# Kernel tuning notes

Measured on AMD Instinct MI355X. Metric: run time of the kernel, lower is better.

The kernel has to match this reference:

```python
import jax, jax.numpy as jnp
import numpy as np

N_NODES = 50000
N_EDGES = 800000
D = 128          # input_dim == output_dim
H = 2 * D        # hidden size = 2*output_dim
EPS = 1e-5       # BatchNorm1d eps


def _mlp(x, W1, b1, g1, beta1, W2, b2):
    # Linear -> BatchNorm1d (training-mode batch stats) -> ReLU -> Linear
    y = x @ W1 + b1
    mu = jnp.mean(y, axis=0)
    var = jnp.mean(jnp.square(y - mu), axis=0)  # biased var, as used for normalization
    y = (y - mu) * jax.lax.rsqrt(var + EPS) * g1 + beta1
    y = jax.nn.relu(y)
    return y @ W2 + b2


def setup_inputs() -> dict:
    key = jax.random.key(0)
    ks = jax.random.split(key, 16)
    h = jax.random.normal(ks[0], (N_NODES, D), dtype=jnp.float32)
    e = jax.random.normal(ks[1], (N_EDGES, D), dtype=jnp.float32)
    src = jax.random.randint(ks[2], (N_EDGES,), 0, N_NODES, dtype=jnp.int32)
    dst = jax.random.randint(ks[3], (N_EDGES,), 0, N_NODES, dtype=jnp.int32)

    def lin(k, fan_in, fan_out):
        return jax.random.normal(k, (fan_in, fan_out), dtype=jnp.float32) * (1.0 / np.sqrt(fan_in))

    params = {
        # mlp_bond: in 2D -> H -> D
        'W1b': lin(ks[4], 2 * D, H), 'b1b': jnp.zeros((H,), jnp.float32),
        'g1b': jnp.ones((H,), jnp.float32), 'beta1b': jnp.zeros((H,), jnp.float32),
        'W2b': lin(ks[5], H, D), 'b2b': jnp.zeros((D,), jnp.float32),
        # mlp_atom: in 2D -> H -> D
        'W1a': lin(ks[6], 2 * D, H), 'b1a': jnp.zeros((H,), jnp.float32),
        'g1a': jnp.ones((H,), jnp.float32), 'beta1a': jnp.zeros((H,), jnp.float32),
        'W2a': lin(ks[7], H, D), 'b2a': jnp.zeros((D,), jnp.float32),
    }
    return {'h': h, 'e': e, 'src': src, 'dst': dst, **params}


def reference(h, e, src, dst,
              W1b, b1b, g1b, beta1b, W2b, b2b,
              W1a, b1a, g1a, beta1a, W2a, b2a):
    # --- bond update: gather u_add_v, concat with e, MLP ---
    sum_h_edge = h[src] + h[dst]                              # [E, D]
    e_new = _mlp(jnp.concatenate([sum_h_edge, e], axis=-1),
                 W1b, b1b, g1b, beta1b, W2b, b2b)             # [E, D]

    # --- atom update: scatter-sum of src node feats and NEW edge feats to dst ---
    sum_h = jax.ops.segment_sum(h[src], dst, num_segments=N_NODES)   # copy_u + sum
    sum_e = jax.ops.segment_sum(e_new, dst, num_segments=N_NODES)   # copy_e + sum
    h_new = _mlp(jnp.concatenate([sum_h, sum_e], axis=-1),
                 W1a, b1a, g1a, beta1a, W2a, b2a)             # [N, D]

    # out_batch_norm=False, out_activation=None, residual=False, dropout=None
    return h_new, e_new
```

## Files before the change

### kernel.cpp

```cpp
#include <hip/hip_runtime.h>
#include <hip/hip_bf16.h>
#include <stdint.h>

#define DD 128
#define HH 256
#define EPSBN 1e-5f

typedef __attribute__((ext_vector_type(4))) float f32x4;
typedef __attribute__((ext_vector_type(8))) short s16x8;
typedef __attribute__((ext_vector_type(4))) short s16x4;

__device__ __forceinline__ unsigned short f2bf(float f){
  union { __hip_bfloat16 h; unsigned short u; } v;
  v.h = __float2bfloat16(f);
  return v.u;
}
__device__ __forceinline__ float bf2f(unsigned short s){
  union{unsigned u; float f;} v; v.u=((unsigned)s)<<16; return v.f;
}
__device__ __forceinline__ int swz(int row, int kb){ return row*512 + (kb ^ ((row&31)<<4)); }

__global__ void wt_kernel(const float* __restrict__ W1b, const float* __restrict__ W2b,
                          const float* __restrict__ W1a, const float* __restrict__ W2a,
                          unsigned short* __restrict__ WT1b, unsigned short* __restrict__ WT2b,
                          unsigned short* __restrict__ WT1a, unsigned short* __restrict__ WT2a){
  int idx = blockIdx.x*256 + threadIdx.x;
  if (idx < 65536){ int n=idx>>8, k=idx&255; WT1b[n*256+k]=f2bf(W1b[k*256+n]); }
  else if (idx < 98304){ int t=idx-65536; int n=t>>8, k=t&255; WT2b[n*256+k]=f2bf(W2b[k*128+n]); }
  else if (idx < 163840){ int t=idx-98304; int n=t>>8, k=t&255; WT1a[n*256+k]=f2bf(W1a[k*256+n]); }
  else if (idx < 196608){ int t=idx-163840; int n=t>>8, k=t&255; WT2a[n*256+k]=f2bf(W2a[k*128+n]); }
}

__global__ void h2bf_hist_kernel(const float* __restrict__ h, unsigned short* __restrict__ hb, int n8,
                                 const int* __restrict__ dst, int* __restrict__ counts, int E){
  int i = blockIdx.x*256 + threadIdx.x;
  if (i < n8){
    f32x4 a = *(const f32x4*)(h + (size_t)i*8);
    f32x4 b = *(const f32x4*)(h + (size_t)i*8 + 4);
    s16x8 p;
    #pragma unroll
    for (int q=0;q<4;q++){ p[q]=(short)f2bf(a[q]); p[4+q]=(short)f2bf(b[q]); }
    *(s16x8*)(hb + (size_t)i*8) = p;
  }
  if (i < E) atomicAdd(&counts[dst[i]], 1);
}

__global__ void scan_kernel(const int* __restrict__ counts, int* __restrict__ offsets,
                            int* __restrict__ cursor, int n){
  __shared__ int wsum[16];
  int tid = threadIdx.x, lane = tid&63, wid = tid>>6;
  int carry = 0;
  int nch = (n + 1023)/1024;
  for (int ch=0; ch<nch; ch++){
    int i = ch*1024 + tid;
    int v = (i<n)? counts[i] : 0;
    int s = v;
    #pragma unroll
    for (int off=1; off<64; off<<=1){ int t = __shfl_up(s, off); if (lane>=off) s += t; }
    if (lane==63) wsum[wid] = s;
    __syncthreads();
    int woff = 0, tot = 0;
    #pragma unroll
    for (int w=0; w<16; w++){ int t = wsum[w]; if (w<wid) woff += t; tot += t; }
    if (i<n){ int excl = carry + woff + s - v; offsets[i]=excl; cursor[i]=excl; }
    carry += tot;
    __syncthreads();
  }
  if (tid==0) offsets[n] = carry;
}

__global__ void fill_kernel(const int* __restrict__ dst, const int* __restrict__ srcv,
                            int* __restrict__ cursor,
                            int* __restrict__ eids, int* __restrict__ esrc, int E){
  int i = blockIdx.x*256 + threadIdx.x;
  if (i < E){
    int slot = atomicAdd(&cursor[dst[i]], 1);
    eids[slot] = i;
    esrc[slot] = srcv[i];
  }
}

__device__ __forceinline__ void gemm1_core(char* xt, const s16x8 (&Bf)[8][2],
                                           float bias0, float bias1,
                                           unsigned short* __restrict__ yout,
                                           float* __restrict__ stats,
                                           int base, int nrows)
{
  const int tid = threadIdx.x;
  const int l = tid&63, w = tid>>6, lr = l&15, lg = l>>4;
  const int nb = w*32;
  f32x4 acc[4][2];
  #pragma unroll
  for (int mt=0;mt<4;mt++)
    #pragma unroll
    for (int nt=0;nt<2;nt++) acc[mt][nt] = (f32x4){0.f,0.f,0.f,0.f};
  #pragma unroll
  for (int kc=0;kc<8;kc++){
    s16x8 af[4];
    #pragma unroll
    for (int mt=0;mt<4;mt++)
      af[mt] = *(const s16x8*)(xt + swz(mt*16 + lr, kc*64 + lg*16));
    #pragma unroll
    for (int nt=0;nt<2;nt++)
      #pragma unroll
      for (int mt=0;mt<4;mt++)
        acc[mt][nt] = __builtin_amdgcn_mfma_f32_16x16x32_bf16(af[mt], Bf[kc][nt], acc[mt][nt], 0,0,0);
  }
  float st1a=0.f, st1b=0.f, st2a=0.f, st2b=0.f;
  #pragma unroll
  for (int mt=0;mt<4;mt++)
    #pragma unroll
    for (int q=0;q<4;q++){
      float m = (base + mt*16 + lg*4 + q < nrows) ? 1.0f : 0.0f;
      float v0 = (acc[mt][0][q] + bias0)*m;
      float v1 = (acc[mt][1][q] + bias1)*m;
      st1a += v0; st2a += v0*v0;
      st1b += v1; st2b += v1*v1;
    }
  __syncthreads();
  #pragma unroll
  for (int mt=0;mt<4;mt++)
    #pragma unroll
    for (int q=0;q<4;q++){
      *(unsigned short*)(xt + (mt*16 + lg*4 + q)*512 + (nb + lr)*2)      = f2bf(acc[mt][0][q] + bias0);
      *(unsigned short*)(xt + (mt*16 + lg*4 + q)*512 + (nb + 16 + lr)*2) = f2bf(acc[mt][1][q] + bias1);
    }
  __syncthreads();
  #pragma unroll
  for (int it=0;it<4;it++){
    int off = it*8192 + tid*16;
    int row = off >> 9;
    if (base + row < nrows)
      *(s16x8*)((char*)yout + (size_t)base*512 + off) = *(const s16x8*)(xt + off);
  }
  {
    int rep = blockIdx.x & 63;
    float s;
    s = st1a; s += __shfl_xor(s,16); s += __shfl_xor(s,32);
    if (l < 16) atomicAdd(&stats[rep*512 + nb + lr], s);
    s = st2a; s += __shfl_xor(s,16); s += __shfl_xor(s,32);
    if (l < 16) atomicAdd(&stats[rep*512 + 256 + nb + lr], s);
    s = st1b; s += __shfl_xor(s,16); s += __shfl_xor(s,32);
    if (l < 16) atomicAdd(&stats[rep*512 + nb + 16 + lr], s);
    s = st2b; s += __shfl_xor(s,16); s += __shfl_xor(s,32);
    if (l < 16) atomicAdd(&stats[rep*512 + 256 + nb + 16 + lr], s);
  }
}

__global__ __launch_bounds__(512, 4) void edge_mlp1(
    const unsigned short* __restrict__ hb, const float* __restrict__ e,
    const int* __restrict__ src, const int* __restrict__ dstv,
    const unsigned short* __restrict__ WT1, const float* __restrict__ b1,
    unsigned short* __restrict__ yout, float* __restrict__ stats, int E)
{
  __shared__ alignas(16) char xt[32768];
  const int tid = threadIdx.x;
  const int l = tid&63, w = tid>>6, lr = l&15, lg = l>>4;
  const int nb = w*32;
  const int base = blockIdx.x*64;

  {
    const int cb = tid&31, r0 = tid>>5;
    #pragma unroll
    for (int k=0;k<4;k++){
      int r = r0 + k*16;
      f32x4 v = *(const f32x4*)(e + (size_t)(base+r)*DD + cb*4);
      s16x4 p;
      #pragma unroll
      for (int q=0;q<4;q++) p[q] = (short)f2bf(v[q]);
      *(s16x4*)(xt + swz(r, 256 + cb*8)) = p;
    }
  }
  {
    const int r = tid>>3, jj = tid&7;
    const int ei = base + r;
    int s_ = src[ei], d_ = dstv[ei];
    const s16x8* hs = (const s16x8*)(hb + (size_t)s_*DD) + jj*2;
    const s16x8* hd = (const s16x8*)(hb + (size_t)d_*DD) + jj*2;
    s16x8 a0=hs[0], a1=hs[1], c0=hd[0], c1=hd[1];
    s16x8 o0, o1;
    #pragma unroll
    for (int q=0;q<8;q++){
      o0[q] = (short)f2bf(bf2f((unsigned short)a0[q]) + bf2f((unsigned short)c0[q]));
      o1[q] = (short)f2bf(bf2f((unsigned short)a1[q]) + bf2f((unsigned short)c1[q]));
    }
    *(s16x8*)(xt + swz(r, jj*32))      = o0;
    *(s16x8*)(xt + swz(r, jj*32 + 16)) = o1;
  }
  s16x8 Bf[8][2];
  #pragma unroll
  for (int kc=0;kc<8;kc++)
    #pragma unroll
    for (int nt=0;nt<2;nt++)
      Bf[kc][nt] = *(const s16x8*)(WT1 + (size_t)(nb + nt*16 + lr)*256 + kc*32 + lg*8);
  float bias0 = b1[nb+lr], bias1 = b1[nb+16+lr];
  __syncthreads();
  gemm1_core(xt, Bf, bias0, bias1, yout, stats, base, E);
}

__global__ __launch_bounds__(256, 8) void node_gather(
    const unsigned short* __restrict__ hb, const float* __restrict__ enew,
    const int* __restrict__ offsets, const int* __restrict__ eids, const int* __restrict__ esrc,
    unsigned short* __restrict__ xnode, int NN)
{
  const int tid = threadIdx.x;
  const int r = tid>>3, jj = tid&7;
  const int node = blockIdx.x*32 + r;
  if (node >= NN) return;
  float ah[16], ae[16];
  #pragma unroll
  for (int q=0;q<16;q++){ ah[q]=0.f; ae[q]=0.f; }
  int beg = offsets[node], end = offsets[node+1];
  if (beg < end){
    int eid = eids[beg];
    int s_  = esrc[beg];
    for (int p = beg; p < end; p++){
      int pn = (p+1 < end) ? p+1 : p;
      int eid_n = eids[pn];
      int s_n   = esrc[pn];
      const s16x8* hs = (const s16x8*)(hb + (size_t)s_*DD + jj*16);
      const f32x4* ep = (const f32x4*)(enew + (size_t)eid*DD + jj*16);
      s16x8 a0 = hs[0], a1 = hs[1];
      f32x4 e0 = ep[0], e1 = ep[1], e2 = ep[2], e3 = ep[3];
      #pragma unroll
      for (int q=0;q<8;q++){ ah[q] += bf2f((unsigned short)a0[q]); ah[8+q] += bf2f((unsigned short)a1[q]); }
      #pragma unroll
      for (int q=0;q<4;q++){ ae[q] += e0[q]; ae[4+q] += e1[q]; ae[8+q] += e2[q]; ae[12+q] += e3[q]; }
      eid = eid_n; s_ = s_n;
    }
  }
  s16x8 o0, o1;
  #pragma unroll
  for (int q=0;q<8;q++){ o0[q] = (short)f2bf(ah[q]); o1[q] = (short)f2bf(ah[8+q]); }
  *(s16x8*)(xnode + (size_t)node*HH + jj*16)     = o0;
  *(s16x8*)(xnode + (size_t)node*HH + jj*16 + 8) = o1;
  #pragma unroll
  for (int q=0;q<8;q++){ o0[q] = (short)f2bf(ae[q]); o1[q] = (short)f2bf(ae[8+q]); }
  *(s16x8*)(xnode + (size_t)node*HH + 128 + jj*16)     = o0;
  *(s16x8*)(xnode + (size_t)node*HH + 128 + jj*16 + 8) = o1;
}

__global__ __launch_bounds__(512, 4) void node_gemm1(
    const unsigned short* __restrict__ xnode,
    const unsigned short* __restrict__ WT1, const float* __restrict__ b1,
    unsigned short* __restrict__ yout, float* __restrict__ stats, int NN)
{
  __shared__ alignas(16) char xt[32768];
  const int tid = threadIdx.x;
  const int l = tid&63, w = tid>>6, lr = l&15, lg = l>>4;
  const int nb = w*32;
  const int base = blockIdx.x*64;

  #pragma unroll
  for (int it=0;it<4;it++){
    int off = it*8192 + tid*16;
    int row = off >> 9, kb = off & 511;
    s16x8 v = {0,0,0,0,0,0,0,0};
    if (base + row < NN) v = *(const s16x8*)((const char*)xnode + (size_t)base*512 + off);
    *(s16x8*)(xt + swz(row, kb)) = v;
  }
  s16x8 Bf[8][2];
  #pragma unroll
  for (int kc=0;kc<8;kc++)
    #pragma unroll
    for (int nt=0;nt<2;nt++)
      Bf[kc][nt] = *(const s16x8*)(WT1 + (size_t)(nb + nt*16 + lr)*256 + kc*32 + lg*8);
  float bias0 = b1[nb+lr], bias1 = b1[nb+16+lr];
  __syncthreads();
  gemm1_core(xt, Bf, bias0, bias1, yout, stats, base, NN);
}

__global__ void finalize_kernel(const float* __restrict__ stats, const float* __restrict__ g,
                                const float* __restrict__ beta, float* __restrict__ scale, float invcnt){
  __shared__ float red[512];
  int tid = threadIdx.x;
  float s = 0.f;
  for (int rep=0; rep<64; rep++) s += stats[rep*512 + tid];
  red[tid] = s;
  __syncthreads();
  if (tid < 256){
    float mu  = red[tid]*invcnt;
    float var = red[256+tid]*invcnt - mu*mu;
    float a = g[tid] * rsqrtf(var + EPSBN);
    float c = beta[tid] - mu*a;
    scale[2*tid] = a; scale[2*tid+1] = c;
  }
}

__global__ __launch_bounds__(512, 4) void mlp2_kernel(const unsigned short* y,
    const unsigned short* __restrict__ WT2, const float* __restrict__ b2,
    const float* __restrict__ scale, float* outp, int nrows)
{
  __shared__ alignas(16) char xt[32768];
  const int tid = threadIdx.x;
  const int l = tid&63, w = tid>>6, lr = l&15, lg = l>>4;
  const int nb = w*16;
  const int base0 = blockIdx.x*128;

  s16x8 Bf[8];
  #pragma unroll
  for (int kc=0;kc<8;kc++)
    Bf[kc] = *(const s16x8*)(WT2 + (size_t)(nb + lr)*HH + kc*32 + lg*8);
  float bias = b2[nb+lr];
  const int cb = tid&31, r0 = tid>>5;
  float sa[8], sc[8];
  #pragma unroll
  for (int q=0;q<8;q++){ sa[q]=scale[2*(cb*8+q)]; sc[q]=scale[2*(cb*8+q)+1]; }

  #pragma unroll 1
  for (int t=0;t<2;t++){
    const int base = base0 + t*64;
    #pragma unroll
    for (int k=0;k<4;k++){
      int r = r0 + k*16;
      s16x8 raw = {0,0,0,0,0,0,0,0};
      if (base + r < nrows) raw = *(const s16x8*)(y + (size_t)(base+r)*HH + cb*8);
      s16x8 o;
      #pragma unroll
      for (int q=0;q<8;q++){
        float f = fmaxf(bf2f((unsigned short)raw[q])*sa[q] + sc[q], 0.0f);
        o[q] = (short)f2bf(f);
      }
      *(s16x8*)(xt + swz(r, cb*16)) = o;
    }
    __syncthreads();
    f32x4 acc[4];
    #pragma unroll
    for (int mt=0;mt<4;mt++) acc[mt] = (f32x4){0.f,0.f,0.f,0.f};
    #pragma unroll
    for (int kc=0;kc<8;kc++){
      s16x8 af[4];
      #pragma unroll
      for (int mt=0;mt<4;mt++)
        af[mt] = *(const s16x8*)(xt + swz(mt*16 + lr, kc*64 + lg*16));
      #pragma unroll
      for (int mt=0;mt<4;mt++)
        acc[mt] = __builtin_amdgcn_mfma_f32_16x16x32_bf16(af[mt], Bf[kc], acc[mt], 0,0,0);
    }
    __syncthreads();
    #pragma unroll
    for (int mt=0;mt<4;mt++)
      #pragma unroll
      for (int q=0;q<4;q++)
        *(float*)(xt + (mt*16 + lg*4 + q)*512 + (nb + lr)*4) = acc[mt][q] + bias;
    __syncthreads();
    #pragma unroll
    for (int it=0;it<4;it++){
      int off = it*8192 + tid*16;
      int row = off >> 9;
      if (base + row < nrows)
        *(f32x4*)(outp + (size_t)(base+row)*DD + ((off&511)>>2)) = *(const f32x4*)(xt + off);
    }
    if (t==0) __syncthreads();
  }
}

extern "C" void kernel_launch(void* const* d_in, const int* in_sizes, int n_in,
                              void* d_out, int out_size, void* d_ws, size_t ws_size,
                              hipStream_t stream) {
  const float* h    = (const float*)d_in[0];
  const float* e    = (const float*)d_in[1];
  const int*   src  = (const int*)d_in[2];
  const int*   dst  = (const int*)d_in[3];
  const float* W1b  = (const float*)d_in[4];
  const float* b1b  = (const float*)d_in[5];
  const float* g1b  = (const float*)d_in[6];
  const float* beta1b=(const float*)d_in[7];
  const float* W2b  = (const float*)d_in[8];
  const float* b2b  = (const float*)d_in[9];
  const float* W1a  = (const float*)d_in[10];
  const float* b1a  = (const float*)d_in[11];
  const float* g1a  = (const float*)d_in[12];
  const float* beta1a=(const float*)d_in[13];
  const float* W2a  = (const float*)d_in[14];
  const float* b2a  = (const float*)d_in[15];

  const int E  = in_sizes[2];
  const int NN = in_sizes[0] / DD;

  char* ws = (char*)d_ws;
  unsigned short* WT1b = (unsigned short*)(ws + 0);
  unsigned short* WT2b = (unsigned short*)(ws + 131072);
  unsigned short* WT1a = (unsigned short*)(ws + 196608);
  unsigned short* WT2a = (unsigned short*)(ws + 327680);
  float* scaleE = (float*)(ws + 393216);
  float* scaleN = (float*)(ws + 395264);
  float* statsE = (float*)(ws + 397312);
  float* statsN = (float*)(ws + 528384);
  int* counts  = (int*)(ws + 659456);
  int* offsets = (int*)(ws + 860160);
  int* cursor  = (int*)(ws + 1060864);
  int* eids    = (int*)(ws + 1261568);
  unsigned short* ya = (unsigned short*)(ws + 4461568);
  unsigned short* hb = (unsigned short*)(ws + 30086144);
  int* esrc   = (int*)(ws + 42886144);

  float* outH = (float*)d_out;
  float* outE = outH + (size_t)NN * DD;
  unsigned short* yE = (unsigned short*)outE;
  unsigned short* xnode = (unsigned short*)outH;

  hipMemsetAsync(ws + 397312, 0, 131072 + 131072 + 200704, stream);

  wt_kernel<<<768, 256, 0, stream>>>(W1b, W2b, W1a, W2a, WT1b, WT2b, WT1a, WT2a);
  h2bf_hist_kernel<<<(NN*DD/8 + 255)/256, 256, 0, stream>>>(h, hb, NN*DD/8, dst, counts, E);
  scan_kernel<<<1, 1024, 0, stream>>>(counts, offsets, cursor, NN);
  fill_kernel<<<(E+255)/256, 256, 0, stream>>>(dst, src, cursor, eids, esrc, E);

  const int tE64  = E/64;
  const int tE128 = E/128;
  const int tN64  = (NN + 63)/64;
  const int tN128 = (NN + 127)/128;
  const int gG    = (NN + 31)/32;

  edge_mlp1<<<tE64, 512, 0, stream>>>(hb, e, src, dst, WT1b, b1b, yE, statsE, E);
  finalize_kernel<<<1, 512, 0, stream>>>(statsE, g1b, beta1b, scaleE, 1.0f/(float)E);
  mlp2_kernel<<<tE128, 512, 0, stream>>>(yE, WT2b, b2b, scaleE, outE, E);
  node_gather<<<gG, 256, 0, stream>>>(hb, outE, offsets, eids, esrc, xnode, NN);
  node_gemm1<<<tN64, 512, 0, stream>>>(xnode, WT1a, b1a, ya, statsN, NN);
  finalize_kernel<<<1, 512, 0, stream>>>(statsN, g1a, beta1a, scaleN, 1.0f/(float)NN);
  mlp2_kernel<<<tN128, 512, 0, stream>>>(ya, WT2a, b2a, scaleN, outH, NN);
}
```

Measured before the change: 841.6 us.

## Fuse node gather into node GEMM1 and hoist edge loads earlier

Merges the node segment-sum gather with the first node GEMM, so the aggregated features go straight into shared memory instead of a bf16 round trip through global memory, and one launch is dropped. In edge_mlp1, the e-tile and gathered h loads are all issued before any conversion, to overlap memory latency. The cost is that the fused kernel uses 512-thread blocks of 64 nodes, which may lower occupancy for the latency-bound gather loop compared with the old 256-thread gather kernel.

```diff
diff --git a/kernel.cpp b/kernel.cpp
--- a/kernel.cpp
+++ b/kernel.cpp
@@ -159,25 +159,28 @@
   const int nb = w*32;
   const int base = blockIdx.x*64;
 
+  const int r = tid>>3, jj = tid&7;
+  const int ei = base + r;
+  int s_ = src[ei], d_ = dstv[ei];
+
+  const int cb = tid&31, r0 = tid>>5;
+  f32x4 ev[4];
+  #pragma unroll
+  for (int k=0;k<4;k++)
+    ev[k] = *(const f32x4*)(e + (size_t)(base + r0 + k*16)*DD + cb*4);
+
+  const s16x8* hs = (const s16x8*)(hb + (size_t)s_*DD) + jj*2;
+  const s16x8* hd = (const s16x8*)(hb + (size_t)d_*DD) + jj*2;
+  s16x8 a0=hs[0], a1=hs[1], c0=hd[0], c1=hd[1];
+
+  #pragma unroll
+  for (int k=0;k<4;k++){
+    s16x4 p;
+    #pragma unroll
+    for (int q=0;q<4;q++) p[q] = (short)f2bf(ev[k][q]);
+    *(s16x4*)(xt + swz(r0 + k*16, 256 + cb*8)) = p;
+  }
   {
-    const int cb = tid&31, r0 = tid>>5;
-    #pragma unroll
-    for (int k=0;k<4;k++){
-      int r = r0 + k*16;
-      f32x4 v = *(const f32x4*)(e + (size_t)(base+r)*DD + cb*4);
-      s16x4 p;
-      #pragma unroll
-      for (int q=0;q<4;q++) p[q] = (short)f2bf(v[q]);
-      *(s16x4*)(xt + swz(r, 256 + cb*8)) = p;
-    }
-  }
-  {
-    const int r = tid>>3, jj = tid&7;
-    const int ei = base + r;
-    int s_ = src[ei], d_ = dstv[ei];
-    const s16x8* hs = (const s16x8*)(hb + (size_t)s_*DD) + jj*2;
-    const s16x8* hd = (const s16x8*)(hb + (size_t)d_*DD) + jj*2;
-    s16x8 a0=hs[0], a1=hs[1], c0=hd[0], c1=hd[1];
     s16x8 o0, o1;
     #pragma unroll
     for (int q=0;q<8;q++){
@@ -198,50 +201,9 @@
   gemm1_core(xt, Bf, bias0, bias1, yout, stats, base, E);
 }
 
-__global__ __launch_bounds__(256, 8) void node_gather(
+__global__ __launch_bounds__(512, 4) void node_mlp1(
     const unsigned short* __restrict__ hb, const float* __restrict__ enew,
     const int* __restrict__ offsets, const int* __restrict__ eids, const int* __restrict__ esrc,
-    unsigned short* __restrict__ xnode, int NN)
-{
-  const int tid = threadIdx.x;
-  const int r = tid>>3, jj = tid&7;
-  const int node = blockIdx.x*32 + r;
-  if (node >= NN) return;
-  float ah[16], ae[16];
-  #pragma unroll
-  for (int q=0;q<16;q++){ ah[q]=0.f; ae[q]=0.f; }
-  int beg = offsets[node], end = offsets[node+1];
-  if (beg < end){
-    int eid = eids[beg];
-    int s_  = esrc[beg];
-    for (int p = beg; p < end; p++){
-      int pn = (p+1 < end) ? p+1 : p;
-      int eid_n = eids[pn];
-      int s_n   = esrc[pn];
-      const s16x8* hs = (const s16x8*)(hb + (size_t)s_*DD + jj*16);
-      const f32x4* ep = (const f32x4*)(enew + (size_t)eid*DD + jj*16);
-      s16x8 a0 = hs[0], a1 = hs[1];
-      f32x4 e0 = ep[0], e1 = ep[1], e2 = ep[2], e3 = ep[3];
-      #pragma unroll
-      for (int q=0;q<8;q++){ ah[q] += bf2f((unsigned short)a0[q]); ah[8+q] += bf2f((unsigned short)a1[q]); }
-      #pragma unroll
-      for (int q=0;q<4;q++){ ae[q] += e0[q]; ae[4+q] += e1[q]; ae[8+q] += e2[q]; ae[12+q] += e3[q]; }
-      eid = eid_n; s_ = s_n;
-    }
-  }
-  s16x8 o0, o1;
-  #pragma unroll
-  for (int q=0;q<8;q++){ o0[q] = (short)f2bf(ah[q]); o1[q] = (short)f2bf(ah[8+q]); }
-  *(s16x8*)(xnode + (size_t)node*HH + jj*16)     = o0;
-  *(s16x8*)(xnode + (size_t)node*HH + jj*16 + 8) = o1;
-  #pragma unroll
-  for (int q=0;q<8;q++){ o0[q] = (short)f2bf(ae[q]); o1[q] = (short)f2bf(ae[8+q]); }
-  *(s16x8*)(xnode + (size_t)node*HH + 128 + jj*16)     = o0;
-  *(s16x8*)(xnode + (size_t)node*HH + 128 + jj*16 + 8) = o1;
-}
-
-__global__ __launch_bounds__(512, 4) void node_gemm1(
-    const unsigned short* __restrict__ xnode,
     const unsigned short* __restrict__ WT1, const float* __restrict__ b1,
     unsigned short* __restrict__ yout, float* __restrict__ stats, int NN)
 {
@@ -250,14 +212,43 @@
   const int l = tid&63, w = tid>>6, lr = l&15, lg = l>>4;
   const int nb = w*32;
   const int base = blockIdx.x*64;
-
-  #pragma unroll
-  for (int it=0;it<4;it++){
-    int off = it*8192 + tid*16;
-    int row = off >> 9, kb = off & 511;
-    s16x8 v = {0,0,0,0,0,0,0,0};
-    if (base + row < NN) v = *(const s16x8*)((const char*)xnode + (size_t)base*512 + off);
-    *(s16x8*)(xt + swz(row, kb)) = v;
+  const int r = tid>>3, jj = tid&7;
+  const int node = base + r;
+
+  float ah[16], ae[16];
+  #pragma unroll
+  for (int q=0;q<16;q++){ ah[q]=0.f; ae[q]=0.f; }
+  if (node < NN){
+    int beg = offsets[node], end = offsets[node+1];
+    if (beg < end){
+      int eid = eids[beg];
+      int s_  = esrc[beg];
+      for (int p = beg; p < end; p++){
+        int pn = (p+1 < end) ? p+1 : p;
+        int eid_n = eids[pn];
+        int s_n   = esrc[pn];
+        const s16x8* hsp = (const s16x8*)(hb + (size_t)s_*DD + jj*16);
+        const f32x4* ep = (const f32x4*)(enew + (size_t)eid*DD + jj*16);
+        s16x8 a0 = hsp[0], a1 = hsp[1];
+        f32x4 e0 = ep[0], e1 = ep[1], e2 = ep[2], e3 = ep[3];
+        #pragma unroll
+        for (int q=0;q<8;q++){ ah[q] += bf2f((unsigned short)a0[q]); ah[8+q] += bf2f((unsigned short)a1[q]); }
+        #pragma unroll
+        for (int q=0;q<4;q++){ ae[q] += e0[q]; ae[4+q] += e1[q]; ae[8+q] += e2[q]; ae[12+q] += e3[q]; }
+        eid = eid_n; s_ = s_n;
+      }
+    }
+  }
+  {
+    s16x8 o0, o1;
+    #pragma unroll
+    for (int q=0;q<8;q++){ o0[q] = (short)f2bf(ah[q]); o1[q] = (short)f2bf(ah[8+q]); }
+    *(s16x8*)(xt + swz(r, jj*32))      = o0;
+    *(s16x8*)(xt + swz(r, jj*32 + 16)) = o1;
+    #pragma unroll
+    for (int q=0;q<8;q++){ o0[q] = (short)f2bf(ae[q]); o1[q] = (short)f2bf(ae[8+q]); }
+    *(s16x8*)(xt + swz(r, 256 + jj*32))      = o0;
+    *(s16x8*)(xt + swz(r, 256 + jj*32 + 16)) = o1;
   }
   s16x8 Bf[8][2];
   #pragma unroll
@@ -398,7 +389,6 @@
   float* outH = (float*)d_out;
   float* outE = outH + (size_t)NN * DD;
   unsigned short* yE = (unsigned short*)outE;
-  unsigned short* xnode = (unsigned short*)outH;
 
   hipMemsetAsync(ws + 397312, 0, 131072 + 131072 + 200704, stream);
 
@@ -411,13 +401,11 @@
   const int tE128 = E/128;
   const int tN64  = (NN + 63)/64;
   const int tN128 = (NN + 127)/128;
-  const int gG    = (NN + 31)/32;
 
   edge_mlp1<<<tE64, 512, 0, stream>>>(hb, e, src, dst, WT1b, b1b, yE, statsE, E);
   finalize_kernel<<<1, 512, 0, stream>>>(statsE, g1b, beta1b, scaleE, 1.0f/(float)E);
   mlp2_kernel<<<tE128, 512, 0, stream>>>(yE, WT2b, b2b, scaleE, outE, E);
-  node_gather<<<gG, 256, 0, stream>>>(hb, outE, offsets, eids, esrc, xnode, NN);
-  node_gemm1<<<tN64, 512, 0, stream>>>(xnode, WT1a, b1a, ya, statsN, NN);
+  node_mlp1<<<tN64, 512, 0, stream>>>(hb, outE, offsets, eids, esrc, WT1a, b1a, ya, statsN, NN);
   finalize_kernel<<<1, 512, 0, stream>>>(statsN, g1a, beta1a, scaleN, 1.0f/(float)NN);
   mlp2_kernel<<<tN128, 512, 0, stream>>>(ya, WT2a, b2a, scaleN, outH, NN);
 }
```

Result: faster. 776.2 us (median of 2 runs) (-7.8%).
